# Optimization experiments

Hardware: AMD Instinct MI355X
Metric: run time of the kernel (lower is better)

The kernel has to match this reference:

```python
import jax, jax.numpy as jnp
import numpy as np

TEMPERATURE = 0.1
BASE_TEMPERATURE = 1.0
LAMBDA_CTR = 1.0
NUM_CLASS = 12
N_VIEWS = 2
EPS_NORM = 1e-12   # F.normalize eps
EPS_POS = 1e-6     # denominator eps on mask.sum


def _graph():
    # binarized tridiagonal AU adjacency (adjacent_matrix after > pcc_threshold -> 1)
    i = jnp.arange(NUM_CLASS)
    return (jnp.abs(i[:, None] - i[None, :]) <= 1).astype(jnp.float32)


def setup_inputs() -> dict:
    key = jax.random.key(0)
    k1, k2 = jax.random.split(key)
    B, d = 512, 4096
    features = jax.random.normal(k1, (B, N_VIEWS, NUM_CLASS, d), dtype=jnp.float32)
    outputs = jax.random.normal(k2, (B, NUM_CLASS), dtype=jnp.float32)
    targets = jax.random.randint(jax.random.fold_in(key, 7), (B, NUM_CLASS), 0, 2, dtype=jnp.int32)
    return {"outputs": outputs, "targets": targets, "features": features}


def reference(outputs, targets, features):
    B = features.shape[0]
    M = N_VIEWS * NUM_CLASS  # anchors per sample
    # per-sample feature rows, L2 normalized (F.normalize, dim=1)
    f = features.reshape(B, M, -1)
    f = f / jnp.clip(jnp.linalg.norm(f, axis=-1, keepdims=True), EPS_NORM)
    # cosine-similarity logits / temperature: [B, M, M]
    logits = jnp.einsum('bmd,bnd->bmn', f, f) / TEMPERATURE
    logits_mask = 1.0 - jnp.eye(M, dtype=jnp.float32)      # drop self-contrast
    mask = jnp.tile(_graph(), (N_VIEWS, N_VIEWS)) * logits_mask  # positives
    # masked log-softmax denominator (is_stable=False: no max subtraction)
    exp_logits = jnp.exp(logits) * logits_mask
    log_prob = logits - jnp.log(exp_logits.sum(-1, keepdims=True))
    mean_log_prob_pos = (mask * log_prob).sum(-1) / (mask.sum(-1) + EPS_POS)  # [B, M]
    per_sample = (-(TEMPERATURE / BASE_TEMPERATURE) * mean_log_prob_pos).mean(-1)  # [B]
    return LAMBDA_CTR * per_sample.sum() / B
```

## Files before the change

### kernel.cpp

```cpp
#include <hip/hip_runtime.h>
#include <math.h>


#define MROWS 24
#define DIM   4096
#define CH    256
#define NCH   (DIM / CH)
#define DEPTH 3
#define PPW   75

typedef float f32x4 __attribute__((ext_vector_type(4)));

constexpr int pair_i(int p) {
    int i = 0;
    while (p >= MROWS - i) { p -= MROWS - i; ++i; }
    return i;
}
constexpr int pair_j(int p) {
    int i = 0;
    while (p >= MROWS - i) { p -= MROWS - i; ++i; }
    return i + p;
}

__device__ __forceinline__ void gll16(const float* g, float* l) {
    __builtin_amdgcn_global_load_lds(
        (const __attribute__((address_space(1))) unsigned int*)g,
        (__attribute__((address_space(3))) unsigned int*)l, 16, 0, 0);
}

#define WAITV(N) do { \
    asm volatile("s_waitcnt vmcnt(" #N ")" ::: "memory"); \
    __builtin_amdgcn_sched_barrier(0); \
} while (0)

template<int W, int P>
__device__ __forceinline__ void accum_pairs(const f32x4* f, float* acc) {
    if constexpr (P < PPW) {
        constexpr int gp = W * PPW + P;
        constexpr int i = pair_i(gp);
        constexpr int j = pair_j(gp);
        #pragma unroll
        for (int s = 0; s < 4; ++s)
            acc[P] = fmaf(f[i][s], f[j][s], acc[P]);
        accum_pairs<W, P + 1>(f, acc);
    }
}

template<int W>
__device__ __forceinline__ void accum_chunk(const float* tile, int lane, float* acc) {
    f32x4 f[MROWS];
    #pragma unroll
    for (int r = 0; r < MROWS; ++r)
        f[r] = *(const f32x4*)(tile + r * CH + lane * 4);
    accum_pairs<W, 0>(f, acc);
}

__global__ __launch_bounds__(256, 2)
void brc_loss_kernel(const float* __restrict__ F, float* __restrict__ out, float scale) {
    __shared__ float tile[DEPTH][MROWS * CH];
    __shared__ float Gf[MROWS * MROWS];
    __shared__ float inv_n[MROWS];
    __shared__ float rowv[MROWS];

    const int tid  = threadIdx.x;
    const int lane = tid & 63;
    const int wave = tid >> 6;
    const float* base = F + (size_t)blockIdx.x * (MROWS * DIM);

    float acc[PPW];
    #pragma unroll
    for (int p = 0; p < PPW; ++p) acc[p] = 0.0f;

    auto issue = [&](int k) {
        const float* src = base + k * CH + lane * 4;
        float* dst = &tile[k % DEPTH][0];
        #pragma unroll
        for (int q = 0; q < 6; ++q) {
            const int r = wave * 6 + q;
            gll16(src + (size_t)r * DIM, dst + r * CH);
        }
    };

    issue(0); issue(1); issue(2);

    #pragma unroll 1
    for (int k = 0; k < NCH; ++k) {
        if (k < NCH - 2)       WAITV(12);
        else if (k == NCH - 2) WAITV(6);
        else                   WAITV(0);
        __builtin_amdgcn_s_barrier();
        __builtin_amdgcn_sched_barrier(0);

        const float* t = &tile[k % DEPTH][0];
        switch (wave) {
            case 0:  accum_chunk<0>(t, lane, acc); break;
            case 1:  accum_chunk<1>(t, lane, acc); break;
            case 2:  accum_chunk<2>(t, lane, acc); break;
            default: accum_chunk<3>(t, lane, acc); break;
        }
        __builtin_amdgcn_sched_barrier(0);
        __builtin_amdgcn_s_barrier();
        if (k + DEPTH < NCH) issue(k + DEPTH);
    }

    #pragma unroll
    for (int p = 0; p < PPW; ++p) {
        float v = acc[p];
        #pragma unroll
        for (int off = 32; off; off >>= 1)
            v += __shfl_xor(v, off, 64);
        if (lane == 0) {
            int gp = wave * PPW + p;
            int i = 0, rem = gp;
            while (rem >= MROWS - i) { rem -= MROWS - i; ++i; }
            int j = i + rem;
            Gf[i * MROWS + j] = v;
            Gf[j * MROWS + i] = v;
        }
    }
    __syncthreads();

    if (tid < MROWS)
        inv_n[tid] = 1.0f / fmaxf(sqrtf(Gf[tid * MROWS + tid]), 1e-12f);
    __syncthreads();

    if (tid < MROWS) {
        const int i = tid;
        const int ci = i % 12;
        const float inv_i = inv_n[i];
        float denom = 0.0f, possum = 0.0f;
        int cnt = 0;
        for (int j = 0; j < MROWS; ++j) {
            if (j == i) continue;
            float l = Gf[i * MROWS + j] * inv_i * inv_n[j] * (1.0f / 0.1f);
            denom += expf(l);
            int cj = j % 12;
            int dc = ci - cj; if (dc < 0) dc = -dc;
            if (dc <= 1) { possum += l; ++cnt; }
        }
        float mean = (possum - (float)cnt * logf(denom)) / ((float)cnt + 1e-6f);
        rowv[i] = -0.1f * mean;
    }
    __syncthreads();

    if (tid == 0) {
        float s = 0.0f;
        #pragma unroll
        for (int i = 0; i < MROWS; ++i) s += rowv[i];
        atomicAdd(out, s * scale);
    }
}

extern "C" void kernel_launch(void* const* d_in, const int* in_sizes, int n_in,
                              void* d_out, int out_size, void* d_ws, size_t ws_size,
                              hipStream_t stream) {
    (void)n_in; (void)d_ws; (void)ws_size; (void)out_size;
    const float* F = (const float*)d_in[2];
    float* out = (float*)d_out;
    const int B = in_sizes[2] / (2 * 12 * DIM);
    const float scale = 1.0f / (24.0f * (float)B);

    hipMemsetAsync(d_out, 0, sizeof(float), stream);
    brc_loss_kernel<<<dim3(B), dim3(256), 0, stream>>>(F, out, scale);
}
```

Before: 335.0 us.

## Use 8 waves per block with column-balanced Gram pair assignment

Doubles the block to 512 threads (8 waves). Each wave now owns three Gram columns (W, W+8, W+16), which gives every wave about 37.5 pairs and cuts accumulator registers so the launch bounds can target 4 blocks per CU. Each wave loads 3 rows per chunk instead of 6. The final butterfly reduction is replaced by a single xor-32 shuffle followed by an LDS transposed reduction across 300 threads, with the reduction buffer reusing the tile memory. This is meant to raise occupancy and memory-level parallelism for the bandwidth-bound load. The cost is more barrier participants, and each wave loads all 24 rows from LDS per chunk instead of holding them in registers.

```diff
diff --git a/kernel.cpp b/kernel.cpp
--- a/kernel.cpp
+++ b/kernel.cpp
@@ -7,20 +7,8 @@
 #define CH    256
 #define NCH   (DIM / CH)
 #define DEPTH 3
-#define PPW   75
 
 typedef float f32x4 __attribute__((ext_vector_type(4)));
-
-constexpr int pair_i(int p) {
-    int i = 0;
-    while (p >= MROWS - i) { p -= MROWS - i; ++i; }
-    return i;
-}
-constexpr int pair_j(int p) {
-    int i = 0;
-    while (p >= MROWS - i) { p -= MROWS - i; ++i; }
-    return i + p;
-}
 
 __device__ __forceinline__ void gll16(const float* g, float* l) {
     __builtin_amdgcn_global_load_lds(
@@ -32,30 +20,80 @@
     asm volatile("s_waitcnt vmcnt(" #N ")" ::: "memory"); \
     __builtin_amdgcn_sched_barrier(0); \
 } while (0)
+#define FENCE() __builtin_amdgcn_sched_barrier(0)
 
-template<int W, int P>
-__device__ __forceinline__ void accum_pairs(const f32x4* f, float* acc) {
-    if constexpr (P < PPW) {
-        constexpr int gp = W * PPW + P;
-        constexpr int i = pair_i(gp);
-        constexpr int j = pair_j(gp);
+__host__ __device__ constexpr int colbase(int W) {
+    return 27 * W + 3 * W * (W - 1) / 2;
+}
+
+template<int W>
+__device__ __forceinline__ void main_loop(const float* base,
+                                          float (*tile)[MROWS * CH],
+                                          float* red, int lane) {
+    constexpr int J0 = W, J1 = W + 8, J2 = W + 16;
+    constexpr int N0 = J0 + 1, N1 = J1 + 1, N2 = J2 + 1;
+    constexpr int ACCN = N0 + N1 + N2;
+
+    float acc[ACCN];
+    #pragma unroll
+    for (int p = 0; p < ACCN; ++p) acc[p] = 0.0f;
+
+    auto issue = [&](int k) {
+        const float* src = base + k * CH + lane * 4;
+        float* dst = &tile[k % DEPTH][0];
         #pragma unroll
-        for (int s = 0; s < 4; ++s)
-            acc[P] = fmaf(f[i][s], f[j][s], acc[P]);
-        accum_pairs<W, P + 1>(f, acc);
+        for (int q = 0; q < 3; ++q) {
+            const int r = 3 * W + q;
+            gll16(src + (size_t)r * DIM, dst + r * CH);
+        }
+    };
+
+    issue(0); issue(1); issue(2);
+
+    #pragma unroll 1
+    for (int k = 0; k < NCH; ++k) {
+        if (k <= NCH - 3)      WAITV(6);
+        else if (k == NCH - 2) WAITV(3);
+        else                   WAITV(0);
+        __builtin_amdgcn_s_barrier();
+        FENCE();
+
+        const float* t = &tile[k % DEPTH][0] + lane * 4;
+        f32x4 f0 = *(const f32x4*)(t + J0 * CH);
+        f32x4 f1 = *(const f32x4*)(t + J1 * CH);
+        f32x4 f2 = *(const f32x4*)(t + J2 * CH);
+        #pragma unroll
+        for (int i = 0; i < MROWS; ++i) {
+            f32x4 fi = *(const f32x4*)(t + i * CH);
+            if (i <= J0) {
+                #pragma unroll
+                for (int e = 0; e < 4; ++e) acc[i] = fmaf(fi[e], f0[e], acc[i]);
+            }
+            if (i <= J1) {
+                #pragma unroll
+                for (int e = 0; e < 4; ++e) acc[N0 + i] = fmaf(fi[e], f1[e], acc[N0 + i]);
+            }
+            if (i <= J2) {
+                #pragma unroll
+                for (int e = 0; e < 4; ++e) acc[N0 + N1 + i] = fmaf(fi[e], f2[e], acc[N0 + N1 + i]);
+            }
+        }
+        FENCE();
+        __builtin_amdgcn_s_barrier();
+        if (k + DEPTH < NCH) issue(k + DEPTH);
+    }
+
+    #pragma unroll
+    for (int p = 0; p < ACCN; ++p)
+        acc[p] += __shfl_xor(acc[p], 32, 64);
+    if (lane < 32) {
+        #pragma unroll
+        for (int p = 0; p < ACCN; ++p)
+            red[(colbase(W) + p) * 32 + lane] = acc[p];
     }
 }
 
-template<int W>
-__device__ __forceinline__ void accum_chunk(const float* tile, int lane, float* acc) {
-    f32x4 f[MROWS];
-    #pragma unroll
-    for (int r = 0; r < MROWS; ++r)
-        f[r] = *(const f32x4*)(tile + r * CH + lane * 4);
-    accum_pairs<W, 0>(f, acc);
-}
-
-__global__ __launch_bounds__(256, 2)
+__global__ __launch_bounds__(512, 4)
 void brc_loss_kernel(const float* __restrict__ F, float* __restrict__ out, float scale) {
     __shared__ float tile[DEPTH][MROWS * CH];
     __shared__ float Gf[MROWS * MROWS];
@@ -66,57 +104,34 @@
     const int lane = tid & 63;
     const int wave = tid >> 6;
     const float* base = F + (size_t)blockIdx.x * (MROWS * DIM);
+    float* red = &tile[0][0];
 
-    float acc[PPW];
-    #pragma unroll
-    for (int p = 0; p < PPW; ++p) acc[p] = 0.0f;
+    switch (wave) {
+        case 0:  main_loop<0>(base, tile, red, lane); break;
+        case 1:  main_loop<1>(base, tile, red, lane); break;
+        case 2:  main_loop<2>(base, tile, red, lane); break;
+        case 3:  main_loop<3>(base, tile, red, lane); break;
+        case 4:  main_loop<4>(base, tile, red, lane); break;
+        case 5:  main_loop<5>(base, tile, red, lane); break;
+        case 6:  main_loop<6>(base, tile, red, lane); break;
+        default: main_loop<7>(base, tile, red, lane); break;
+    }
+    __syncthreads();
 
-    auto issue = [&](int k) {
-        const float* src = base + k * CH + lane * 4;
-        float* dst = &tile[k % DEPTH][0];
+    if (tid < 300) {
+        float s = 0.0f;
         #pragma unroll
-        for (int q = 0; q < 6; ++q) {
-            const int r = wave * 6 + q;
-            gll16(src + (size_t)r * DIM, dst + r * CH);
-        }
-    };
-
-    issue(0); issue(1); issue(2);
-
-    #pragma unroll 1
-    for (int k = 0; k < NCH; ++k) {
-        if (k < NCH - 2)       WAITV(12);
-        else if (k == NCH - 2) WAITV(6);
-        else                   WAITV(0);
-        __builtin_amdgcn_s_barrier();
-        __builtin_amdgcn_sched_barrier(0);
-
-        const float* t = &tile[k % DEPTH][0];
-        switch (wave) {
-            case 0:  accum_chunk<0>(t, lane, acc); break;
-            case 1:  accum_chunk<1>(t, lane, acc); break;
-            case 2:  accum_chunk<2>(t, lane, acc); break;
-            default: accum_chunk<3>(t, lane, acc); break;
-        }
-        __builtin_amdgcn_sched_barrier(0);
-        __builtin_amdgcn_s_barrier();
-        if (k + DEPTH < NCH) issue(k + DEPTH);
-    }
-
-    #pragma unroll
-    for (int p = 0; p < PPW; ++p) {
-        float v = acc[p];
-        #pragma unroll
-        for (int off = 32; off; off >>= 1)
-            v += __shfl_xor(v, off, 64);
-        if (lane == 0) {
-            int gp = wave * PPW + p;
-            int i = 0, rem = gp;
-            while (rem >= MROWS - i) { rem -= MROWS - i; ++i; }
-            int j = i + rem;
-            Gf[i * MROWS + j] = v;
-            Gf[j * MROWS + i] = v;
-        }
+        for (int l = 0; l < 32; ++l)
+            s += red[tid * 32 + ((l + tid) & 31)];
+        int W = 0;
+        while (W < 7 && tid >= colbase(W + 1)) ++W;
+        int p = tid - colbase(W);
+        int i, j;
+        if (p <= W)               { j = W;      i = p; }
+        else if (p <= 2 * W + 9)  { j = W + 8;  i = p - (W + 1); }
+        else                      { j = W + 16; i = p - (2 * W + 10); }
+        Gf[i * MROWS + j] = s;
+        Gf[j * MROWS + i] = s;
     }
     __syncthreads();
 
@@ -161,5 +176,5 @@
     const float scale = 1.0f / (24.0f * (float)B);
 
     hipMemsetAsync(d_out, 0, sizeof(float), stream);
-    brc_loss_kernel<<<dim3(B), dim3(256), 0, stream>>>(F, out, scale);
+    brc_loss_kernel<<<dim3(B), dim3(512), 0, stream>>>(F, out, scale);
 }
```

Measured after the change: 300.7 us. -10.2%, faster.

## Replace LDS-staged Gram accumulation with register-blocked 6x6 group pairs per wave

Applied to the files above, without the earlier changes.

Drops the LDS triple-buffered global_load_lds pipeline. The 24 rows are split into four groups of six, and six waves each compute one cross-group 6x6 block of the Gram matrix plus a third of the diagonal-group triangles. Each wave loads its rows straight into registers, with software double buffering. This removes LDS traffic and block-wide barriers and gives more FMAs per loaded value. In exchange each row is read from global or L2 by three waves, and register pressure rises with 48 vector registers of data plus 50 accumulators.

```diff
diff --git a/kernel.cpp b/kernel.cpp
--- a/kernel.cpp
+++ b/kernel.cpp
@@ -4,60 +4,97 @@
 
 #define MROWS 24
 #define DIM   4096
-#define CH    256
-#define NCH   (DIM / CH)
-#define DEPTH 3
-#define PPW   75
+#define NIT   16
 
 typedef float f32x4 __attribute__((ext_vector_type(4)));
 
-constexpr int pair_i(int p) {
+__device__ __host__ constexpr int tri_i(int p) {
     int i = 0;
-    while (p >= MROWS - i) { p -= MROWS - i; ++i; }
+    while (p >= 6 - i) { p -= 6 - i; ++i; }
     return i;
 }
-constexpr int pair_j(int p) {
+__device__ __host__ constexpr int tri_j(int p) {
     int i = 0;
-    while (p >= MROWS - i) { p -= MROWS - i; ++i; }
+    while (p >= 6 - i) { p -= 6 - i; ++i; }
     return i + p;
 }
 
-__device__ __forceinline__ void gll16(const float* g, float* l) {
-    __builtin_amdgcn_global_load_lds(
-        (const __attribute__((address_space(1))) unsigned int*)g,
-        (__attribute__((address_space(3))) unsigned int*)l, 16, 0, 0);
-}
 
-#define WAITV(N) do { \
-    asm volatile("s_waitcnt vmcnt(" #N ")" ::: "memory"); \
-    __builtin_amdgcn_sched_barrier(0); \
-} while (0)
+template<int GA, int GB, int RA, int RB>
+__device__ __forceinline__ void wave_work(const float* __restrict__ base,
+                                          int lane, float* Gf) {
+    const float* pa = base + (size_t)GA * 6 * DIM + lane * 4;
+    const float* pb = base + (size_t)GB * 6 * DIM + lane * 4;
 
-template<int W, int P>
-__device__ __forceinline__ void accum_pairs(const f32x4* f, float* acc) {
-    if constexpr (P < PPW) {
-        constexpr int gp = W * PPW + P;
-        constexpr int i = pair_i(gp);
-        constexpr int j = pair_j(gp);
+    float acc[50];
+    #pragma unroll
+    for (int p = 0; p < 50; ++p) acc[p] = 0.0f;
+
+    f32x4 A0[6], B0[6], A1[6], B1[6];
+
+    auto load12 = [&](f32x4 (&A)[6], f32x4 (&B)[6], int k) {
+        const int off = k * 256;
         #pragma unroll
-        for (int s = 0; s < 4; ++s)
-            acc[P] = fmaf(f[i][s], f[j][s], acc[P]);
-        accum_pairs<W, P + 1>(f, acc);
+        for (int r = 0; r < 6; ++r) {
+            A[r] = *(const f32x4*)(pa + (size_t)r * DIM + off);
+            B[r] = *(const f32x4*)(pb + (size_t)r * DIM + off);
+        }
+    };
+    auto compute = [&](const f32x4 (&A)[6], const f32x4 (&B)[6]) {
+        #pragma unroll
+        for (int a = 0; a < 6; ++a)
+            #pragma unroll
+            for (int b = 0; b < 6; ++b)
+                #pragma unroll
+                for (int e = 0; e < 4; ++e)
+                    acc[a * 6 + b] = fmaf(A[a][e], B[b][e], acc[a * 6 + b]);
+        #pragma unroll
+        for (int p = 0; p < 7; ++p) {
+            const int q = 3 * p + RA;
+            const int i = tri_i(q), j = tri_j(q);
+            #pragma unroll
+            for (int e = 0; e < 4; ++e)
+                acc[36 + p] = fmaf(A[i][e], A[j][e], acc[36 + p]);
+        }
+        #pragma unroll
+        for (int p = 0; p < 7; ++p) {
+            const int q = 3 * p + RB;
+            const int i = tri_i(q), j = tri_j(q);
+            #pragma unroll
+            for (int e = 0; e < 4; ++e)
+                acc[43 + p] = fmaf(B[i][e], B[j][e], acc[43 + p]);
+        }
+    };
+
+    load12(A0, B0, 0);
+    #pragma unroll 1
+    for (int k = 0; k < NIT; k += 2) {
+        if (k + 1 < NIT) load12(A1, B1, k + 1);
+        compute(A0, B0);
+        if (k + 2 < NIT) load12(A0, B0, k + 2);
+        compute(A1, B1);
+    }
+
+    #pragma unroll
+    for (int p = 0; p < 50; ++p) {
+        float v = acc[p];
+        #pragma unroll
+        for (int off = 32; off; off >>= 1)
+            v += __shfl_xor(v, off, 64);
+        if (lane == 0) {
+            int i, j;
+            if (p < 36)      { i = GA * 6 + p / 6;  j = GB * 6 + p % 6; }
+            else if (p < 43) { int q = 3 * (p - 36) + RA; i = GA * 6 + tri_i(q); j = GA * 6 + tri_j(q); }
+            else             { int q = 3 * (p - 43) + RB; i = GB * 6 + tri_i(q); j = GB * 6 + tri_j(q); }
+            Gf[i * MROWS + j] = v;
+            Gf[j * MROWS + i] = v;
+        }
     }
 }
 
-template<int W>
-__device__ __forceinline__ void accum_chunk(const float* tile, int lane, float* acc) {
-    f32x4 f[MROWS];
-    #pragma unroll
-    for (int r = 0; r < MROWS; ++r)
-        f[r] = *(const f32x4*)(tile + r * CH + lane * 4);
-    accum_pairs<W, 0>(f, acc);
-}
-
-__global__ __launch_bounds__(256, 2)
+__global__ __attribute__((amdgpu_flat_work_group_size(384, 384),
+                          amdgpu_waves_per_eu(3, 3)))
 void brc_loss_kernel(const float* __restrict__ F, float* __restrict__ out, float scale) {
-    __shared__ float tile[DEPTH][MROWS * CH];
     __shared__ float Gf[MROWS * MROWS];
     __shared__ float inv_n[MROWS];
     __shared__ float rowv[MROWS];
@@ -67,56 +104,13 @@
     const int wave = tid >> 6;
     const float* base = F + (size_t)blockIdx.x * (MROWS * DIM);
 
-    float acc[PPW];
-    #pragma unroll
-    for (int p = 0; p < PPW; ++p) acc[p] = 0.0f;
-
-    auto issue = [&](int k) {
-        const float* src = base + k * CH + lane * 4;
-        float* dst = &tile[k % DEPTH][0];
-        #pragma unroll
-        for (int q = 0; q < 6; ++q) {
-            const int r = wave * 6 + q;
-            gll16(src + (size_t)r * DIM, dst + r * CH);
-        }
-    };
-
-    issue(0); issue(1); issue(2);
-
-    #pragma unroll 1
-    for (int k = 0; k < NCH; ++k) {
-        if (k < NCH - 2)       WAITV(12);
-        else if (k == NCH - 2) WAITV(6);
-        else                   WAITV(0);
-        __builtin_amdgcn_s_barrier();
-        __builtin_amdgcn_sched_barrier(0);
-
-        const float* t = &tile[k % DEPTH][0];
-        switch (wave) {
-            case 0:  accum_chunk<0>(t, lane, acc); break;
-            case 1:  accum_chunk<1>(t, lane, acc); break;
-            case 2:  accum_chunk<2>(t, lane, acc); break;
-            default: accum_chunk<3>(t, lane, acc); break;
-        }
-        __builtin_amdgcn_sched_barrier(0);
-        __builtin_amdgcn_s_barrier();
-        if (k + DEPTH < NCH) issue(k + DEPTH);
-    }
-
-    #pragma unroll
-    for (int p = 0; p < PPW; ++p) {
-        float v = acc[p];
-        #pragma unroll
-        for (int off = 32; off; off >>= 1)
-            v += __shfl_xor(v, off, 64);
-        if (lane == 0) {
-            int gp = wave * PPW + p;
-            int i = 0, rem = gp;
-            while (rem >= MROWS - i) { rem -= MROWS - i; ++i; }
-            int j = i + rem;
-            Gf[i * MROWS + j] = v;
-            Gf[j * MROWS + i] = v;
-        }
+    switch (wave) {
+        case 0:  wave_work<0, 1, 0, 0>(base, lane, Gf); break;
+        case 1:  wave_work<0, 2, 1, 0>(base, lane, Gf); break;
+        case 2:  wave_work<0, 3, 2, 0>(base, lane, Gf); break;
+        case 3:  wave_work<1, 2, 1, 1>(base, lane, Gf); break;
+        case 4:  wave_work<1, 3, 2, 1>(base, lane, Gf); break;
+        default: wave_work<2, 3, 2, 2>(base, lane, Gf); break;
     }
     __syncthreads();
 
@@ -161,5 +155,5 @@
     const float scale = 1.0f / (24.0f * (float)B);
 
     hipMemsetAsync(d_out, 0, sizeof(float), stream);
-    brc_loss_kernel<<<dim3(B), dim3(256), 0, stream>>>(F, out, scale);
+    brc_loss_kernel<<<dim3(B), dim3(384), 0, stream>>>(F, out, scale);
 }
```

Result: slower. 822.2 us (+145.5%).
